# Kernel tuning notes

Hardware: AMD Instinct MI355X
Metric: run time of the kernel (lower is better)

## Reference

```python
import jax, jax.numpy as jnp
import numpy as np

B, S, IN, OUT = 4, 2048, 4096, 12288


def setup_inputs() -> dict:
    key = jax.random.key(0)
    k1, k2, k3, k4 = jax.random.split(key, 4)
    x = jax.random.normal(k1, (B, S, IN), dtype=jnp.float32).astype(jnp.float16)
    # int8 quantized weight in [-127, 127]
    w_q = jax.random.randint(k2, (OUT, IN), -127, 128, dtype=jnp.int32).astype(jnp.int8)
    # per-output-channel dequant scale (fp32, positive, small)
    w_scale = (jax.random.uniform(k3, (OUT, 1), dtype=jnp.float32) + 0.5) * 0.01
    bias = (jax.random.normal(k4, (OUT,), dtype=jnp.float32) * 0.02).astype(jnp.float16)
    return {"x": x, "w_q": w_q, "w_scale": w_scale, "bias": bias}


def reference(x, w_q, w_scale, bias):
    # dynamic per-token activation quantization: scale = absmax / 127
    x32 = x.astype(jnp.float32)
    x_scale = jnp.maximum(jnp.max(jnp.abs(x32), axis=-1, keepdims=True), 1e-6) / 127.0  # [B,S,1]
    x_q = jnp.clip(jnp.round(x32 / x_scale), -128, 127).astype(jnp.int8)  # [B,S,IN]
    acc = jnp.einsum("bsi,oi->bso", x_q, w_q, preferred_element_type=jnp.int32)  # [B,S,OUT]
    # fused dequant (per-token scale * per-channel scale) + bias
    out = acc.astype(jnp.float32) * x_scale * w_scale[:, 0]
    out = out + bias.astype(jnp.float32)
    return out.astype(x.dtype)
```

## Files before the change

### kernel.cpp

```cpp
#include <hip/hip_runtime.h>
#include <hip/hip_fp16.h>
#include <stdint.h>

#define M_TOK 8192
#define K_IN  4096
#define N_OUT 12288

typedef int v4i_t __attribute__((ext_vector_type(4)));

__device__ __forceinline__ void load_lds16(const void* g, void* l) {
    __builtin_amdgcn_global_load_lds(
        (const __attribute__((address_space(1))) unsigned int*)g,
        (__attribute__((address_space(3))) unsigned int*)l, 16, 0, 0);
}

#define PACK_BLOCKS 2048
#define PACK_ITERS  24

__global__ __launch_bounds__(256) void prep_kernel(
    const int* __restrict__ wsrc, uint32_t* __restrict__ wdst,
    const float* __restrict__ x, int8_t* __restrict__ xq, float* __restrict__ xs) {
    const int tid = threadIdx.x;
    const int bid = blockIdx.x;
    if (bid < PACK_BLOCKS) {
        size_t i = (size_t)bid * 256 + tid;
#pragma unroll
        for (int it = 0; it < PACK_ITERS; ++it, i += (size_t)PACK_BLOCKS * 256) {
            const int4 v = ((const int4*)wsrc)[i];
            wdst[i] = (uint32_t)(uint8_t)(int8_t)v.x
                    | ((uint32_t)(uint8_t)(int8_t)v.y << 8)
                    | ((uint32_t)(uint8_t)(int8_t)v.z << 16)
                    | ((uint32_t)(uint8_t)(int8_t)v.w << 24);
        }
        return;
    }
    const int token = bid - PACK_BLOCKS;
    const float4* src = (const float4*)(x + (size_t)token * K_IN);
    float v[16];
#pragma unroll
    for (int c = 0; c < 4; ++c) {
        float4 p = src[c * 256 + tid];
        v[c * 4 + 0] = p.x; v[c * 4 + 1] = p.y;
        v[c * 4 + 2] = p.z; v[c * 4 + 3] = p.w;
    }
    float amax = 0.f;
#pragma unroll
    for (int i = 0; i < 16; ++i) amax = fmaxf(amax, fabsf(v[i]));
#pragma unroll
    for (int off = 32; off >= 1; off >>= 1)
        amax = fmaxf(amax, __shfl_xor(amax, off));
    __shared__ float wmax[4];
    const int wave = tid >> 6, lane = tid & 63;
    if (lane == 0) wmax[wave] = amax;
    __syncthreads();
    amax = fmaxf(fmaxf(wmax[0], wmax[1]), fmaxf(wmax[2], wmax[3]));
    const float scale = fmaxf(amax, 1e-6f) / 127.0f;
    if (tid == 0) xs[token] = scale;

    uint32_t* dst = (uint32_t*)(xq + (size_t)token * K_IN);
#pragma unroll
    for (int c = 0; c < 4; ++c) {
        uint32_t w = 0;
#pragma unroll
        for (int e = 0; e < 4; ++e) {
            float r = rintf(v[c * 4 + e] / scale);
            r = fminf(fmaxf(r, -128.f), 127.f);
            w |= (uint32_t)(uint8_t)(int8_t)(int)r << (8 * e);
        }
        dst[c * 256 + tid] = w;
    }
}

__global__ __launch_bounds__(512, 2) void gemm_kernel(
    const int8_t* __restrict__ xq, const float* __restrict__ xs,
    const int8_t* __restrict__ wq, const float* __restrict__ wscale,
    const float* __restrict__ bias, float* __restrict__ out) {
    extern __shared__ char smem[];

    const int tid  = threadIdx.x;
    const int wid  = tid >> 6, lane = tid & 63;
    const int wr   = wid >> 2, wc = wid & 3;

    const int bid = blockIdx.x;
    const int xcd = bid & 7;
    const int s   = bid >> 3;
    const int g   = s >> 5;
    const int r_  = s & 31;
    const int by  = xcd * 4 + (r_ & 3);
    const int bx  = g * 8 + (r_ >> 2);
    const int m0  = by * 256, n0 = bx * 256;

    const int8_t* Ag = xq + (size_t)m0 * K_IN;
    const int8_t* Bg = wq + (size_t)n0 * K_IN;

    const int rl = (lane >> 2) & 15;
    const int rg = (rl & 0xA) | ((rl & 1) << 2) | ((rl >> 2) & 1);
    const size_t rowByte = (size_t)(wid * 16 + rg) * K_IN;
    const int gsw16 = ((lane & 3) ^ ((lane >> 3) & 3)) << 4;

    const int fr = lane & 15, fq = lane >> 4;
    const int sfr = (fr & 0xA) | ((fr & 1) << 2) | ((fr >> 2) & 1);
    const int frOff = sfr * 64 + (((fq ^ (sfr >> 1)) & 3) << 4);

    auto stage_half = [&](int h) {
        const int th = h >> 2, r = h & 3;
        const int isB = r & 1, kk = r >> 1;
        const int8_t* G = isB ? Bg : Ag;
        char* lb = smem + (isB << 16) + ((((th & 1) << 1) | kk) << 14) + (wid << 10);
        const int8_t* g0 = G + rowByte + th * 128 + (kk << 6) + gsw16;
        load_lds16(g0, lb);
        load_lds16(g0 + (size_t)128 * K_IN, lb + 8192);
    };

    v4i_t acc[8][4] = {};

#pragma unroll
    for (int h = 0; h < 5; ++h) stage_half(h);
    asm volatile("s_waitcnt vmcnt(6)" ::: "memory");
    __builtin_amdgcn_sched_barrier(0);
    __builtin_amdgcn_s_barrier();
    __builtin_amdgcn_sched_barrier(0);

    v4i_t af[4], bf[4];

#define PHASE(T_, PH_, LAST_)                                                          \
    {                                                                                  \
        const int kk_   = (PH_) >> 1;                                                  \
        const int slab_ = ((((T_) & 1) << 1) | kk_) << 14;                             \
        const int ioff_ = ((PH_) & 1) * 4;                                             \
        if (((PH_) & 1) == 0) {                                                        \
            _Pragma("unroll")                                                          \
            for (int j = 0; j < 4; ++j)                                                \
                bf[j] = *(const v4i_t*)(smem + 65536 + slab_ + (wc << 12) + frOff + (j << 10)); \
        }                                                                              \
        _Pragma("unroll")                                                              \
        for (int i = 0; i < 4; ++i)                                                    \
            af[i] = *(const v4i_t*)(smem + slab_ + (wr << 13) + frOff + ((ioff_ + i) << 10)); \
        const int hs_ = 4 * (T_) + 5 + (PH_);                                          \
        if (hs_ < 128) stage_half(hs_);                                                \
        __builtin_amdgcn_sched_barrier(0);                                             \
        __builtin_amdgcn_s_barrier();                                                  \
        asm volatile("s_waitcnt lgkmcnt(0)" ::: "memory");                             \
        __builtin_amdgcn_sched_barrier(0);                                             \
        __builtin_amdgcn_s_setprio(1);                                                 \
        _Pragma("unroll")                                                              \
        for (int i = 0; i < 4; ++i)                                                    \
            _Pragma("unroll")                                                          \
            for (int j = 0; j < 4; ++j)                                                \
                acc[ioff_ + i][j] =                                                    \
                    __builtin_amdgcn_mfma_i32_16x16x64_i8(af[i], bf[j], acc[ioff_ + i][j], 0, 0, 0); \
        __builtin_amdgcn_s_setprio(0);                                                 \
        if ((PH_) == 0) {                                                              \
            if (LAST_) asm volatile("s_waitcnt vmcnt(0)" ::: "memory");                \
            else       asm volatile("s_waitcnt vmcnt(4)" ::: "memory");                \
            __builtin_amdgcn_sched_barrier(0);                                         \
        }                                                                              \
        if ((PH_) == 2 && !(LAST_)) {                                                  \
            asm volatile("s_waitcnt vmcnt(4)" ::: "memory");                           \
            __builtin_amdgcn_sched_barrier(0);                                         \
        }                                                                              \
    }

    for (int T = 0; T < 31; ++T) {
        PHASE(T, 0, false)
        PHASE(T, 1, false)
        PHASE(T, 2, false)
        PHASE(T, 3, false)
    }
    PHASE(31, 0, true)
    PHASE(31, 1, true)
    PHASE(31, 2, true)
    PHASE(31, 3, true)
#undef PHASE

    const int col = lane & 15, rq = lane >> 4;
#pragma unroll
    for (int i = 0; i < 8; ++i) {
        const int mb = m0 + wr * 128 + i * 16 + rq * 4;
        float xsv[4];
#pragma unroll
        for (int r = 0; r < 4; ++r) xsv[r] = xs[mb + r];
#pragma unroll
        for (int j = 0; j < 4; ++j) {
            const int n = n0 + wc * 64 + j * 16 + col;
            const float ws = wscale[n];
            const float bv = bias[n];
#pragma unroll
            for (int r = 0; r < 4; ++r) {
                float o = (float)acc[i][j][r] * xsv[r] * ws + bv;
                o = __half2float(__float2half(o));
                out[(size_t)(mb + r) * N_OUT + n] = o;
            }
        }
    }
}

extern "C" void kernel_launch(void* const* d_in, const int* in_sizes, int n_in,
                              void* d_out, int out_size, void* d_ws, size_t ws_size,
                              hipStream_t stream) {
    const float* x      = (const float*)d_in[0];
    const int*   wq32   = (const int*)d_in[1];
    const float* wscale = (const float*)d_in[2];
    const float* bias   = (const float*)d_in[3];
    float* out = (float*)d_out;

    int8_t* xq  = (int8_t*)d_ws;
    float*  xs  = (float*)((char*)d_ws + (size_t)M_TOK * K_IN);
    int8_t* wq8 = (int8_t*)((char*)d_ws + (size_t)M_TOK * K_IN + 65536);

    static bool attrDone = false;
    if (!attrDone) {
        (void)hipFuncSetAttribute((const void*)gemm_kernel,
                                  hipFuncAttributeMaxDynamicSharedMemorySize, 131072);
        attrDone = true;
    }

    prep_kernel<<<PACK_BLOCKS + M_TOK, 256, 0, stream>>>(wq32, (uint32_t*)wq8, x, xq, xs);

    gemm_kernel<<<dim3(1536), dim3(512), 131072, stream>>>(xq, xs, wq8, wscale, bias, out);
}
```

Before: 943.2 us.

## Double-buffer LDS fragment reads to prefetch next phase during MFMAs

Adds two register buffers for the A and B fragments and issues the LDS reads for the next phase before running the current phase's MFMAs. Partial lgkmcnt waits take the place of the full drain, and the workgroup barrier moves to the end of each phase. The goal is to hide LDS read latency behind matrix work. In exchange it uses more VGPRs, and the hand-counted waitcnt values and the LDS slab reuse ordering must stay correct across the relocated barrier.

```diff
diff --git a/kernel.cpp b/kernel.cpp
--- a/kernel.cpp
+++ b/kernel.cpp
@@ -113,6 +113,17 @@
     };
 
     v4i_t acc[8][4] = {};
+    v4i_t af[2][4], bf[2][4];
+
+#define ISSUE_BF(bufb_, slab_)                                                         \
+    _Pragma("unroll")                                                                  \
+    for (int j = 0; j < 4; ++j)                                                        \
+        bf[bufb_][j] = *(const v4i_t*)(smem + 65536 + (slab_) + (wc << 12) + frOff + (j << 10));
+
+#define ISSUE_AF(bufa_, slab_, ioff_)                                                  \
+    _Pragma("unroll")                                                                  \
+    for (int i = 0; i < 4; ++i)                                                        \
+        af[bufa_][i] = *(const v4i_t*)(smem + (slab_) + (wr << 13) + frOff + (((ioff_) + i) << 10));
 
 #pragma unroll
     for (int h = 0; h < 5; ++h) stage_half(h);
@@ -120,35 +131,34 @@
     __builtin_amdgcn_sched_barrier(0);
     __builtin_amdgcn_s_barrier();
     __builtin_amdgcn_sched_barrier(0);
-
-    v4i_t af[4], bf[4];
+    ISSUE_BF(0, 0)
+    ISSUE_AF(0, 0, 0)
 
 #define PHASE(T_, PH_, LAST_)                                                          \
     {                                                                                  \
-        const int kk_   = (PH_) >> 1;                                                  \
-        const int slab_ = ((((T_) & 1) << 1) | kk_) << 14;                             \
-        const int ioff_ = ((PH_) & 1) * 4;                                             \
-        if (((PH_) & 1) == 0) {                                                        \
-            _Pragma("unroll")                                                          \
-            for (int j = 0; j < 4; ++j)                                                \
-                bf[j] = *(const v4i_t*)(smem + 65536 + slab_ + (wc << 12) + frOff + (j << 10)); \
+        if (!((LAST_) && (PH_) == 3)) {                                                \
+            const int nT_   = ((PH_) == 3) ? (T_) + 1 : (T_);                          \
+            const int nPH_  = ((PH_) + 1) & 3;                                         \
+            const int slabN_ = ((((nT_) & 1) << 1) | (nPH_ >> 1)) << 14;               \
+            if ((nPH_ & 1) == 0) { ISSUE_BF(nPH_ >> 1, slabN_) }                       \
+            ISSUE_AF(nPH_ & 1, slabN_, (nPH_ & 1) * 4)                                 \
         }                                                                              \
-        _Pragma("unroll")                                                              \
-        for (int i = 0; i < 4; ++i)                                                    \
-            af[i] = *(const v4i_t*)(smem + slab_ + (wr << 13) + frOff + ((ioff_ + i) << 10)); \
         const int hs_ = 4 * (T_) + 5 + (PH_);                                          \
         if (hs_ < 128) stage_half(hs_);                                                \
-        __builtin_amdgcn_sched_barrier(0);                                             \
-        __builtin_amdgcn_s_barrier();                                                  \
-        asm volatile("s_waitcnt lgkmcnt(0)" ::: "memory");                             \
+        if ((LAST_) && (PH_) == 3)                                                     \
+            asm volatile("s_waitcnt lgkmcnt(0)" ::: "memory");                         \
+        else if (((PH_) & 1) == 1)                                                     \
+            asm volatile("s_waitcnt lgkmcnt(8)" ::: "memory");                         \
+        else                                                                           \
+            asm volatile("s_waitcnt lgkmcnt(4)" ::: "memory");                         \
         __builtin_amdgcn_sched_barrier(0);                                             \
         __builtin_amdgcn_s_setprio(1);                                                 \
         _Pragma("unroll")                                                              \
         for (int i = 0; i < 4; ++i)                                                    \
             _Pragma("unroll")                                                          \
             for (int j = 0; j < 4; ++j)                                                \
-                acc[ioff_ + i][j] =                                                    \
-                    __builtin_amdgcn_mfma_i32_16x16x64_i8(af[i], bf[j], acc[ioff_ + i][j], 0, 0, 0); \
+                acc[((PH_) & 1) * 4 + i][j] = __builtin_amdgcn_mfma_i32_16x16x64_i8(   \
+                    af[(PH_) & 1][i], bf[(PH_) >> 1][j], acc[((PH_) & 1) * 4 + i][j], 0, 0, 0); \
         __builtin_amdgcn_s_setprio(0);                                                 \
         if ((PH_) == 0) {                                                              \
             if (LAST_) asm volatile("s_waitcnt vmcnt(0)" ::: "memory");                \
@@ -159,6 +169,9 @@
             asm volatile("s_waitcnt vmcnt(4)" ::: "memory");                           \
             __builtin_amdgcn_sched_barrier(0);                                         \
         }                                                                              \
+        __builtin_amdgcn_sched_barrier(0);                                             \
+        __builtin_amdgcn_s_barrier();                                                  \
+        __builtin_amdgcn_sched_barrier(0);                                             \
     }
 
     for (int T = 0; T < 31; ++T) {
@@ -172,6 +185,8 @@
     PHASE(31, 2, true)
     PHASE(31, 3, true)
 #undef PHASE
+#undef ISSUE_BF
+#undef ISSUE_AF
 
     const int col = lane & 15, rq = lane >> 4;
 #pragma unroll
```

Measured after the change: 949.7 us. About the same (+0.7%).
